# Kernel tuning notes

Hardware: AMD Instinct MI355X
Metric: run time of the kernel (lower is better)

The kernel has to match this reference:

```python
import jax, jax.numpy as jnp
import numpy as np

TEMPERATURE = 0.07
TOP_MARGIN = 0.95
BOTTOM_MARGIN = 0.05

BATCH = 8192
DIM = 1024


def setup_inputs() -> dict:
    key = jax.random.key(0)
    kA, kB = jax.random.split(key)
    embedding_A = jax.random.normal(kA, (BATCH, DIM), dtype=jnp.float32)
    embedding_B = jax.random.normal(kB, (BATCH, DIM), dtype=jnp.float32)
    return {"embedding_A": embedding_A, "embedding_B": embedding_B}


def _l2norm(x):
    return x * jax.lax.rsqrt(jnp.sum(x * x, axis=-1, keepdims=True))


def reference(embedding_A, embedding_B):
    a = _l2norm(embedding_A)
    b = _l2norm(embedding_B)
    B = a.shape[0]
    sim = a @ b.T                                   # [B, B]
    pos = jnp.diagonal(sim)                         # [B]
    eye = jnp.eye(B, dtype=bool)
    upper = pos[:, None] * TOP_MARGIN
    lower = pos[:, None] * BOTTOM_MARGIN
    neg_mask = (sim <= upper) & (sim >= lower) & ~eye   # [B, B]

    # Per-row CE over [positive, hard negatives] == masked logsumexp - pos/tau.
    z = sim / TEMPERATURE
    full_mask = neg_mask | eye                      # positive always included
    masked = jnp.where(full_mask, z, -jnp.inf)
    m = jnp.max(masked, axis=1, keepdims=True)      # finite: diag always present
    lse = m[:, 0] + jnp.log(jnp.sum(jnp.exp(masked - m), axis=1))
    per_row = lse - pos / TEMPERATURE               # [B]

    valid = jnp.any(neg_mask, axis=1)               # rows with >=1 negative
    count = jnp.sum(valid)
    total = jnp.sum(jnp.where(valid, per_row, 0.0))
    return total / jnp.maximum(count, 1).astype(total.dtype)
```

## Files before the change

### kernel.cpp

```cpp
#include <hip/hip_runtime.h>
#include <hip/hip_bf16.h>

#define BATCH 8192
#define DIM   1024
#define INV_TAU (1.0f / 0.07f)
#define TOPM 0.95f
#define BOTM 0.05f

#define BM 256
#define BN 256
#define BK 64
#define NT (DIM / BK)

typedef __attribute__((ext_vector_type(4))) float f32x4;
typedef __attribute__((ext_vector_type(8))) short bf16x8;

typedef __attribute__((address_space(3))) void       lds_void_t;
typedef const __attribute__((address_space(1))) void gbl_void_t;

__device__ inline void async_copy16(const void* g, void* l) {
    __builtin_amdgcn_global_load_lds((gbl_void_t*)g, (lds_void_t*)l, 16, 0, 0);
}

__device__ inline unsigned short f2bf(float f) {
    __hip_bfloat16 h = __float2bfloat16(f);
    return *reinterpret_cast<unsigned short*>(&h);
}

__global__ __launch_bounds__(256) void prep_kernel(
    const float* __restrict__ A, const float* __restrict__ B,
    unsigned short* __restrict__ An, unsigned short* __restrict__ Bn,
    float* __restrict__ pos, float* __restrict__ S)
{
    int row = blockIdx.x;
    int t = threadIdx.x;
    const float4* a4 = (const float4*)(A + (size_t)row * DIM);
    const float4* b4 = (const float4*)(B + (size_t)row * DIM);
    float4 av = a4[t];
    float4 bv = b4[t];
    float sa = av.x*av.x + av.y*av.y + av.z*av.z + av.w*av.w;
    float sb = bv.x*bv.x + bv.y*bv.y + bv.z*bv.z + bv.w*bv.w;
    float dp = av.x*bv.x + av.y*bv.y + av.z*bv.z + av.w*bv.w;
    #pragma unroll
    for (int d = 32; d > 0; d >>= 1) {
        sa += __shfl_down(sa, d);
        sb += __shfl_down(sb, d);
        dp += __shfl_down(dp, d);
    }
    __shared__ float red[3][4];
    int lane = t & 63, w = t >> 6;
    if (lane == 0) { red[0][w] = sa; red[1][w] = sb; red[2][w] = dp; }
    __syncthreads();
    sa = red[0][0] + red[0][1] + red[0][2] + red[0][3];
    sb = red[1][0] + red[1][1] + red[1][2] + red[1][3];
    dp = red[2][0] + red[2][1] + red[2][2] + red[2][3];
    float ra = rsqrtf(sa);
    float rb = rsqrtf(sb);
    if (t == 0) {
        pos[row] = dp * ra * rb;
        S[row] = 0.0f;
    }
    ushort4 oa, ob;
    oa.x = f2bf(av.x * ra); oa.y = f2bf(av.y * ra);
    oa.z = f2bf(av.z * ra); oa.w = f2bf(av.w * ra);
    ob.x = f2bf(bv.x * rb); ob.y = f2bf(bv.y * rb);
    ob.z = f2bf(bv.z * rb); ob.w = f2bf(bv.w * rb);
    ((ushort4*)(An + (size_t)row * DIM))[t] = oa;
    ((ushort4*)(Bn + (size_t)row * DIM))[t] = ob;
}

__global__ __launch_bounds__(512, 2) void sim_loss_kernel(
    const unsigned short* __restrict__ An, const unsigned short* __restrict__ Bn,
    const float* __restrict__ pos, float* __restrict__ S)
{
    __shared__ char lds[131072];

    int tid  = threadIdx.x;
    int lane = tid & 63;
    int wave = tid >> 6;
    int wm = wave >> 2, wn = wave & 3;
    int fr = lane & 15;
    int q  = lane >> 4;

    int bid = blockIdx.x;
    int swz = (bid & 7) * 128 + (bid >> 3);
    int by = swz >> 5, bx = swz & 31;
    int rowBase = by * BM, colBase = bx * BN;

    f32x4 acc[8][4] = {};
    bf16x8 a[4][2];
    bf16x8 b[2][2][2];

    int sw = (fr & 7) << 4;
    int c0 = (q * 16) ^ sw;
    int c1 = (64 + q * 16) ^ sw;
    int aRow = (wm * 128 + fr) * 128;
    int bRow = (wn * 64 + fr) * 128;

    int strow = tid >> 3;
    int scb   = ((tid & 7) * 16) ^ ((strow & 7) << 4);
    const char* gA = (const char*)An + (size_t)(rowBase + strow) * 2048 + scb;
    const char* gB = (const char*)Bn + (size_t)(colBase + strow) * 2048 + scb;
    int ldst = tid * 16;

#define STAGE(gbase, u, h, ldsdst) do {                                              \
    async_copy16((gbase) + (size_t)(h) * 262144 + (size_t)(u) * 128,                 \
                 (ldsdst) + (h) * 16384 + ldst);                                     \
    async_copy16((gbase) + (size_t)(h) * 262144 + 131072 + (size_t)(u) * 128,        \
                 (ldsdst) + (h) * 16384 + 8192 + ldst);                              \
} while (0)

#define LDA(sAp, mh) do {                                                            \
    _Pragma("unroll") for (int m = 0; m < 4; ++m) {                                  \
        a[m][0] = *(const bf16x8*)((sAp) + aRow + (mh) * 8192 + m * 2048 + c0);      \
        a[m][1] = *(const bf16x8*)((sAp) + aRow + (mh) * 8192 + m * 2048 + c1);      \
    }                                                                                \
} while (0)

#define LDB(sBp, nh) do {                                                            \
    _Pragma("unroll") for (int n = 0; n < 2; ++n) {                                  \
        b[nh][n][0] = *(const bf16x8*)((sBp) + bRow + (nh) * 4096 + n * 2048 + c0);  \
        b[nh][n][1] = *(const bf16x8*)((sBp) + bRow + (nh) * 4096 + n * 2048 + c1);  \
    }                                                                                \
} while (0)

#define MM(mh, nh) do {                                                              \
    _Pragma("unroll") for (int m = 0; m < 4; ++m)                                    \
    _Pragma("unroll") for (int n = 0; n < 2; ++n) {                                  \
        acc[(mh)*4+m][(nh)*2+n] = __builtin_amdgcn_mfma_f32_16x16x32_bf16(           \
            a[m][0], b[nh][n][0], acc[(mh)*4+m][(nh)*2+n], 0, 0, 0);                 \
        acc[(mh)*4+m][(nh)*2+n] = __builtin_amdgcn_mfma_f32_16x16x32_bf16(           \
            a[m][1], b[nh][n][1], acc[(mh)*4+m][(nh)*2+n], 0, 0, 0);                 \
    }                                                                                \
} while (0)

#define SBAR() do { __builtin_amdgcn_sched_barrier(0); __builtin_amdgcn_s_barrier(); \
                    __builtin_amdgcn_sched_barrier(0); } while (0)
#define LGK0() do { asm volatile("s_waitcnt lgkmcnt(0)" ::: "memory");               \
                    __builtin_amdgcn_sched_barrier(0); } while (0)
#define VMC(n) do { asm volatile("s_waitcnt vmcnt(" #n ")" ::: "memory");            \
                    __builtin_amdgcn_sched_barrier(0); } while (0)
#define PRI1() __builtin_amdgcn_s_setprio(1)
#define PRI0() __builtin_amdgcn_s_setprio(0)

#define KTILE(p, uA, uB) do {                                                        \
    const char* sAp = lds + (p) * 32768;                                             \
    const char* sBp = lds + 65536 + (p) * 32768;                                     \
    char* stA = lds + ((p) ^ 1) * 32768;                                             \
    char* stB = lds + 65536 + (p) * 32768;                                           \
     LDA(sAp, 0); LDB(sBp, 0); STAGE(gA, (uA), 0, stA);                      \
    SBAR(); LGK0(); PRI1(); MM(0, 0); PRI0(); SBAR();                                \
     LDB(sBp, 1); STAGE(gA, (uA), 1, stA);                                   \
    SBAR(); LGK0(); PRI1(); MM(0, 1); PRI0(); SBAR();                                \
     LDA(sAp, 1); STAGE(gB, (uB), 0, stB);                                   \
    SBAR(); LGK0(); PRI1(); MM(1, 1); PRI0(); SBAR();                                \
     STAGE(gB, (uB), 1, stB);                                                \
    SBAR(); LGK0(); PRI1(); MM(1, 0); PRI0(); VMC(4); SBAR();                        \
} while (0)

    STAGE(gA, 0, 0, lds);
    STAGE(gA, 0, 1, lds);
    STAGE(gB, 0, 0, lds + 65536);
    STAGE(gB, 0, 1, lds + 65536);
    STAGE(gB, 1, 0, lds + 65536 + 32768);
    STAGE(gB, 1, 1, lds + 65536 + 32768);
    VMC(4);
    SBAR();

    for (int tt = 0; tt < NT / 2; ++tt) {
        int t0 = tt * 2;
        { int uA = (t0 + 1) & 15, uB = (t0 + 2) & 15; KTILE(0, uA, uB); }
        { int uA = (t0 + 2) & 15, uB = (t0 + 3) & 15; KTILE(1, uA, uB); }
    }
    VMC(0);

    #pragma unroll
    for (int m = 0; m < 8; ++m) {
        #pragma unroll
        for (int j = 0; j < 4; ++j) {
            int i = rowBase + wm * 128 + m * 16 + q * 4 + j;
            float p  = pos[i];
            float up = TOPM * p, lo = BOTM * p;
            float rs = 0.0f;
            #pragma unroll
            for (int n = 0; n < 4; ++n) {
                float sv = acc[m][n][j];
                int col = colBase + wn * 64 + n * 16 + fr;
                if (sv <= up && sv >= lo && col != i)
                    rs += __expf((sv - p) * INV_TAU);
            }
            #pragma unroll
            for (int d = 1; d < 16; d <<= 1)
                rs += __shfl_xor(rs, d);
            if (fr == 0 && rs != 0.0f)
                atomicAdd(&S[i], rs);
        }
    }
#undef STAGE
#undef LDA
#undef LDB
#undef MM
#undef SBAR
#undef LGK0
#undef VMC
#undef PRI1
#undef PRI0
#undef KTILE
}

__global__ __launch_bounds__(256) void finalize_kernel(
    const float* __restrict__ S, float* __restrict__ out)
{
    int t = threadIdx.x;
    float tot = 0.0f;
    int c = 0;
    for (int i = t; i < BATCH; i += 256) {
        float s = S[i];
        if (s > 0.0f) { tot += log1pf(s); c += 1; }
    }
    #pragma unroll
    for (int d = 32; d > 0; d >>= 1) {
        tot += __shfl_down(tot, d);
        c   += __shfl_down(c, d);
    }
    __shared__ float st[4];
    __shared__ int   sc[4];
    int lane = t & 63, w = t >> 6;
    if (lane == 0) { st[w] = tot; sc[w] = c; }
    __syncthreads();
    if (t == 0) {
        float T = st[0] + st[1] + st[2] + st[3];
        int   C = sc[0] + sc[1] + sc[2] + sc[3];
        out[0] = T / (float)(C > 0 ? C : 1);
    }
}

extern "C" void kernel_launch(void* const* d_in, const int* in_sizes, int n_in,
                              void* d_out, int out_size, void* d_ws, size_t ws_size,
                              hipStream_t stream) {
    const float* A = (const float*)d_in[0];
    const float* B = (const float*)d_in[1];

    char* ws = (char*)d_ws;
    unsigned short* An = (unsigned short*)ws;
    unsigned short* Bn = An + (size_t)BATCH * DIM;
    float* pos = (float*)(Bn + (size_t)BATCH * DIM);
    float* S   = pos + BATCH;
    float* out = (float*)d_out;

    prep_kernel<<<BATCH, 256, 0, stream>>>(A, B, An, Bn, pos, S);
    sim_loss_kernel<<<dim3(BATCH / BM * BATCH / BN / 1), 512, 0, stream>>>(An, Bn, pos, S);
    finalize_kernel<<<1, 256, 0, stream>>>(S, out);
}
```

Before: 249.2 us.

## Remap tiles per XCD for L2 locality and relax barriers in K-loop

Replaces the block-index swizzle with a mapping that gives each XCD a compact 4x8 patch of output tiles inside quadrant generations, so blocks sharing an XCD L2 reuse the same A and B rows. The K-loop schedule is loosened: redundant barriers and sched_barriers are removed, the B fragment loads are issued together with partial lgkmcnt waits, and the final vmcnt wait moves after the epilogue. This aims to cut L2 misses and synchronization stalls, but risks LDS read/write hazards if the remaining barriers do not fully order staging writes against reads.

After: 212.5 us. -14.7%, faster.

```diff
diff --git a/kernel.cpp b/kernel.cpp
--- a/kernel.cpp
+++ b/kernel.cpp
@@ -83,8 +83,10 @@
     int q  = lane >> 4;
 
     int bid = blockIdx.x;
-    int swz = (bid & 7) * 128 + (bid >> 3);
-    int by = swz >> 5, bx = swz & 31;
+    int xcd = bid & 7, idx = bid >> 3, gen = idx >> 5, j = idx & 31;
+    int qr = gen >> 1, qc = (gen & 1) ^ (qr & 1);
+    int by = qr * 16 + (xcd >> 1) * 4 + (j >> 3);
+    int bx = qc * 16 + (xcd & 1) * 8 + (j & 7);
     int rowBase = by * BM, colBase = bx * BN;
 
     f32x4 acc[8][4] = {};
@@ -134,12 +136,11 @@
     }                                                                                \
 } while (0)
 
-#define SBAR() do { __builtin_amdgcn_sched_barrier(0); __builtin_amdgcn_s_barrier(); \
-                    __builtin_amdgcn_sched_barrier(0); } while (0)
-#define LGK0() do { asm volatile("s_waitcnt lgkmcnt(0)" ::: "memory");               \
-                    __builtin_amdgcn_sched_barrier(0); } while (0)
-#define VMC(n) do { asm volatile("s_waitcnt vmcnt(" #n ")" ::: "memory");            \
-                    __builtin_amdgcn_sched_barrier(0); } while (0)
+#define BAR() __builtin_amdgcn_s_barrier()
+#define SCH() __builtin_amdgcn_sched_barrier(0)
+#define LGKM(n) do { asm volatile("s_waitcnt lgkmcnt(" #n ")" ::: "memory");         \
+                     SCH(); } while (0)
+#define VMC(n)  asm volatile("s_waitcnt vmcnt(" #n ")" ::: "memory")
 #define PRI1() __builtin_amdgcn_s_setprio(1)
 #define PRI0() __builtin_amdgcn_s_setprio(0)
 
@@ -148,14 +149,18 @@
     const char* sBp = lds + 65536 + (p) * 32768;                                     \
     char* stA = lds + ((p) ^ 1) * 32768;                                             \
     char* stB = lds + 65536 + (p) * 32768;                                           \
-     LDA(sAp, 0); LDB(sBp, 0); STAGE(gA, (uA), 0, stA);                      \
-    SBAR(); LGK0(); PRI1(); MM(0, 0); PRI0(); SBAR();                                \
-     LDB(sBp, 1); STAGE(gA, (uA), 1, stA);                                   \
-    SBAR(); LGK0(); PRI1(); MM(0, 1); PRI0(); SBAR();                                \
-     LDA(sAp, 1); STAGE(gB, (uB), 0, stB);                                   \
-    SBAR(); LGK0(); PRI1(); MM(1, 1); PRI0(); SBAR();                                \
-     STAGE(gB, (uB), 1, stB);                                                \
-    SBAR(); LGK0(); PRI1(); MM(1, 0); PRI0(); VMC(4); SBAR();                        \
+                             \
+    LDA(sAp, 0); LDB(sBp, 0); LDB(sBp, 1); STAGE(gA, (uA), 0, stA);                  \
+    LGKM(4); PRI1(); MM(0, 0); PRI0(); BAR();                                        \
+                                                                    \
+    STAGE(gA, (uA), 1, stA);                                                         \
+    LGKM(0); PRI1(); MM(0, 1); PRI0(); BAR(); SCH();                                 \
+                                                               \
+    LDA(sAp, 1); STAGE(gB, (uB), 0, stB);                                            \
+    LGKM(0); PRI1(); MM(1, 1); PRI0(); BAR();                                        \
+                                       \
+    STAGE(gB, (uB), 1, stB);                                                         \
+    PRI1(); MM(1, 0); PRI0(); VMC(4); BAR(); SCH();                                  \
 } while (0)
 
     STAGE(gA, 0, 0, lds);
@@ -165,26 +170,26 @@
     STAGE(gB, 1, 0, lds + 65536 + 32768);
     STAGE(gB, 1, 1, lds + 65536 + 32768);
     VMC(4);
-    SBAR();
+    BAR();
+    SCH();
 
     for (int tt = 0; tt < NT / 2; ++tt) {
         int t0 = tt * 2;
         { int uA = (t0 + 1) & 15, uB = (t0 + 2) & 15; KTILE(0, uA, uB); }
         { int uA = (t0 + 2) & 15, uB = (t0 + 3) & 15; KTILE(1, uA, uB); }
     }
-    VMC(0);
 
     #pragma unroll
     for (int m = 0; m < 8; ++m) {
         #pragma unroll
-        for (int j = 0; j < 4; ++j) {
-            int i = rowBase + wm * 128 + m * 16 + q * 4 + j;
+        for (int j2 = 0; j2 < 4; ++j2) {
+            int i = rowBase + wm * 128 + m * 16 + q * 4 + j2;
             float p  = pos[i];
             float up = TOPM * p, lo = BOTM * p;
             float rs = 0.0f;
             #pragma unroll
             for (int n = 0; n < 4; ++n) {
-                float sv = acc[m][n][j];
+                float sv = acc[m][n][j2];
                 int col = colBase + wn * 64 + n * 16 + fr;
                 if (sv <= up && sv >= lo && col != i)
                     rs += __expf((sv - p) * INV_TAU);
@@ -196,12 +201,14 @@
                 atomicAdd(&S[i], rs);
         }
     }
+    VMC(0);
 #undef STAGE
 #undef LDA
 #undef LDB
 #undef MM
-#undef SBAR
-#undef LGK0
+#undef BAR
+#undef SCH
+#undef LGKM
 #undef VMC
 #undef PRI1
 #undef PRI0
@@ -249,6 +256,6 @@
     float* out = (float*)d_out;
 
     prep_kernel<<<BATCH, 256, 0, stream>>>(A, B, An, Bn, pos, S);
-    sim_loss_kernel<<<dim3(BATCH / BM * BATCH / BN / 1), 512, 0, stream>>>(An, Bn, pos, S);
+    sim_loss_kernel<<<dim3(BATCH / BM * BATCH / BN), 512, 0, stream>>>(An, Bn, pos, S);
     finalize_kernel<<<1, 256, 0, stream>>>(S, out);
 }
```
